# Kernel optimization log

Measured on AMD Instinct MI355X. Metric: run time of the kernel, lower is better.

## Reference

```python
import jax, jax.numpy as jnp
import numpy as np

B, S, D = 1, 4096, 512
QK_DIM, N_HEADS = 512, 8
HEAD_DIM = QK_DIM // N_HEADS


def setup_inputs() -> dict:
    key = jax.random.key(0)
    ks = jax.random.split(key, 9)
    s_in = 1.0 / np.sqrt(D)
    s_v = 1.0 / np.sqrt(QK_DIM)
    return {
        "x": jax.random.normal(ks[0], (B, S, D), dtype=jnp.float32),
        # torch nn.Linear convention: weight (out_features, in_features)
        "Wq": jax.random.uniform(ks[1], (QK_DIM, D), jnp.float32, -s_in, s_in),
        "bq": jax.random.uniform(ks[2], (QK_DIM,), jnp.float32, -s_in, s_in),
        "Wk": jax.random.uniform(ks[3], (QK_DIM, D), jnp.float32, -s_in, s_in),
        "bk": jax.random.uniform(ks[4], (QK_DIM,), jnp.float32, -s_in, s_in),
        "Wv": jax.random.uniform(ks[5], (QK_DIM, D), jnp.float32, -s_in, s_in),
        "bv": jax.random.uniform(ks[6], (QK_DIM,), jnp.float32, -s_in, s_in),
        "Wo": jax.random.uniform(ks[7], (D, QK_DIM), jnp.float32, -s_v, s_v),
        "bo": jax.random.uniform(ks[8], (D,), jnp.float32, -s_v, s_v),
    }


def reference(x, Wq, bq, Wk, bk, Wv, bv, Wo, bo):
    # Faithful to source: tokens flattened over batch*seq before head split.
    n = x.shape[0] * x.shape[1]  # B*S
    Q = (x @ Wq.T + bq).reshape(n, N_HEADS, HEAD_DIM).transpose(1, 0, 2)  # (H, N, hd)
    K = (x @ Wk.T + bk).reshape(n, N_HEADS, HEAD_DIM).transpose(1, 0, 2)
    V = (x @ Wv.T + bv).reshape(n, N_HEADS, HEAD_DIM).transpose(1, 0, 2)
    scores = jnp.einsum("hnd,hmd->hnm", Q, K) / np.sqrt(HEAD_DIM).astype(np.float32)
    attn = jax.nn.softmax(scores, axis=-1)                # (H, N, N) materialized
    ctx = jnp.einsum("hnm,hmd->hnd", attn, V)             # (H, N, hd)
    ctx = ctx.transpose(1, 0, 2).reshape(n, QK_DIM)       # (N, qk_dim)
    return ctx @ Wo.T + bo                                # (N, input_dim)
```

## Files before the change

kernel.cpp:

```cpp
#include <hip/hip_runtime.h>
#include <math.h>

#define N_TOK 4096
#define DMODEL 512
#define NH 8
#define HD 64

typedef __attribute__((ext_vector_type(4))) float f32x4;
typedef __attribute__((ext_vector_type(8))) _Float16 f16x8;
typedef __attribute__((ext_vector_type(4))) _Float16 f16x4;

#define MFMA16(A, B, C) __builtin_amdgcn_mfma_f32_16x16x32_f16(A, B, C, 0, 0, 0)

__global__ __launch_bounds__(256) void cast_x(const float* __restrict__ x,
                                              _Float16* __restrict__ X16) {
    int i = (blockIdx.x * 256 + threadIdx.x) * 8;
    f32x4 a = *(const f32x4*)&x[i];
    f32x4 b = *(const f32x4*)&x[i + 4];
    f16x8 o = {(_Float16)a[0], (_Float16)a[1], (_Float16)a[2], (_Float16)a[3],
               (_Float16)b[0], (_Float16)b[1], (_Float16)b[2], (_Float16)b[3]};
    *(f16x8*)&X16[i] = o;
}

__global__ __launch_bounds__(768) void qkv_gemm(const _Float16* __restrict__ X16,
                                                const float* __restrict__ Wq,
                                                const float* __restrict__ bq,
                                                const float* __restrict__ Wk,
                                                const float* __restrict__ bk,
                                                const float* __restrict__ Wv,
                                                const float* __restrict__ bv,
                                                _Float16* __restrict__ Q16,
                                                _Float16* __restrict__ K16,
                                                _Float16* __restrict__ VT16) {
    __shared__ __align__(16) _Float16 smem[46080];
    _Float16* AsB = smem;
    _Float16* WsB = smem + 18432;

    int t = threadIdx.x;
    int w = t >> 6, l = t & 63, quad = l >> 4, ln = l & 15;
    int z = w >> 2, ww = w & 3;
    int n0 = blockIdx.x * 128, o0 = blockIdx.y * 64;
    int h = o0 >> 6;

    const float* biasz = (z == 0) ? bq : (z == 1) ? bk : bv;

    f32x4 acc[2][4] = {};

    bool isA = (t < 256);
    int asr = t >> 3, asc = (t & 7) * 8;
    int tt = t - 256;
    int wr = tt >> 3, wc = (tt & 7) * 8;

    const _Float16* Abase = X16 + (size_t)n0 * DMODEL;
    const float* W0 = Wq + (size_t)o0 * DMODEL;
    const float* W1 = Wk + (size_t)o0 * DMODEL;
    const float* W2 = Wv + (size_t)o0 * DMODEL;

    f16x8 pa[4];
    f32x4 pw[3][2];
    if (isA) {
#pragma unroll
        for (int r = 0; r < 4; r++)
            pa[r] = *(const f16x8*)&Abase[(size_t)(asr + r * 32) * DMODEL + asc];
    } else {
        pw[0][0] = *(const f32x4*)&W0[(size_t)wr * DMODEL + wc];
        pw[0][1] = *(const f32x4*)&W0[(size_t)wr * DMODEL + wc + 4];
        pw[1][0] = *(const f32x4*)&W1[(size_t)wr * DMODEL + wc];
        pw[1][1] = *(const f32x4*)&W1[(size_t)wr * DMODEL + wc + 4];
        pw[2][0] = *(const f32x4*)&W2[(size_t)wr * DMODEL + wc];
        pw[2][1] = *(const f32x4*)&W2[(size_t)wr * DMODEL + wc + 4];
    }

    for (int it = 0; it < 8; it++) {
        int p = it & 1;
        if (isA) {
#pragma unroll
            for (int r = 0; r < 4; r++)
                *(f16x8*)&AsB[(size_t)(p * 128 + asr + r * 32) * 72 + asc] = pa[r];
        } else {
#pragma unroll
            for (int zt = 0; zt < 3; zt++) {
                f16x8 wv_ = {(_Float16)pw[zt][0][0], (_Float16)pw[zt][0][1],
                             (_Float16)pw[zt][0][2], (_Float16)pw[zt][0][3],
                             (_Float16)pw[zt][1][0], (_Float16)pw[zt][1][1],
                             (_Float16)pw[zt][1][2], (_Float16)pw[zt][1][3]};
                *(f16x8*)&WsB[(size_t)((p * 3 + zt) * 64 + wr) * 72 + wc] = wv_;
            }
        }
        __syncthreads();

        int k1 = (it + 1) * 64;
        if (k1 < DMODEL) {
            if (isA) {
#pragma unroll
                for (int r = 0; r < 4; r++)
                    pa[r] = *(const f16x8*)&Abase[(size_t)(asr + r * 32) * DMODEL + k1 + asc];
            } else {
                pw[0][0] = *(const f32x4*)&W0[(size_t)wr * DMODEL + k1 + wc];
                pw[0][1] = *(const f32x4*)&W0[(size_t)wr * DMODEL + k1 + wc + 4];
                pw[1][0] = *(const f32x4*)&W1[(size_t)wr * DMODEL + k1 + wc];
                pw[1][1] = *(const f32x4*)&W1[(size_t)wr * DMODEL + k1 + wc + 4];
                pw[2][0] = *(const f32x4*)&W2[(size_t)wr * DMODEL + k1 + wc];
                pw[2][1] = *(const f32x4*)&W2[(size_t)wr * DMODEL + k1 + wc + 4];
            }
        }

#pragma unroll
        for (int ks = 0; ks < 2; ks++) {
            f16x8 af0 = *(const f16x8*)&AsB[(size_t)(p * 128 + ww * 32 + ln) * 72 +
                                            ks * 32 + quad * 8];
            f16x8 af1 = *(const f16x8*)&AsB[(size_t)(p * 128 + ww * 32 + 16 + ln) * 72 +
                                            ks * 32 + quad * 8];
#pragma unroll
            for (int c = 0; c < 4; c++) {
                f16x8 bf = *(const f16x8*)&WsB[(size_t)((p * 3 + z) * 64 + c * 16 + ln) * 72 +
                                               ks * 32 + quad * 8];
                acc[0][c] = MFMA16(af0, bf, acc[0][c]);
                acc[1][c] = MFMA16(af1, bf, acc[1][c]);
            }
        }
    }

    __syncthreads();

    const float QS = 0.125f * 1.44269504088896340736f;
    _Float16* Qs = smem;
    _Float16* Ksep = smem + 9216;
    _Float16* Vt = smem + 18432;

    if (z < 2) {
        _Float16* st = (z == 0) ? Qs : Ksep;
        float sc_ = (z == 0) ? QS : 1.0f;
#pragma unroll
        for (int c = 0; c < 4; c++) {
            float bv_ = biasz[o0 + c * 16 + ln];
#pragma unroll
            for (int rt = 0; rt < 2; rt++)
#pragma unroll
                for (int i = 0; i < 4; i++) {
                    int lr = ww * 32 + rt * 16 + quad * 4 + i;
                    st[(size_t)lr * 72 + c * 16 + ln] =
                        (_Float16)((acc[rt][c][i] + bv_) * sc_);
                }
        }
    } else {
#pragma unroll
        for (int c = 0; c < 4; c++) {
            float bv_ = biasz[o0 + c * 16 + ln];
#pragma unroll
            for (int rt = 0; rt < 2; rt++)
#pragma unroll
                for (int i = 0; i < 4; i++) {
                    int np = (ww >> 1) * 64 + (quad * 4 + i) * 4 + (ww & 1) * 2 + rt;
                    Vt[(size_t)(c * 16 + ln) * 136 + np] = (_Float16)(acc[rt][c][i] + bv_);
                }
        }
    }
    __syncthreads();

    if (t < 256) {
#pragma unroll
        for (int k = 0; k < 4; k++) {
            int row = k * 32 + (t >> 3), col = (t & 7) * 8;
            *(f16x8*)&Q16[((size_t)h * N_TOK + n0 + row) * HD + col] =
                *(const f16x8*)&Qs[(size_t)row * 72 + col];
        }
    } else if (t < 512) {
        int u = t - 256;
#pragma unroll
        for (int k = 0; k < 4; k++) {
            int row = k * 32 + (u >> 3), col = (u & 7) * 8;
            *(f16x8*)&K16[((size_t)h * N_TOK + n0 + row) * HD + col] =
                *(const f16x8*)&Ksep[(size_t)row * 72 + col];
        }
    } else {
        int u = t - 512;
#pragma unroll
        for (int k = 0; k < 4; k++) {
            int d = k * 16 + (u >> 4), col = (u & 15) * 8;
            *(f16x8*)&VT16[((size_t)h * HD + d) * N_TOK + n0 + col] =
                *(const f16x8*)&Vt[(size_t)d * 136 + col];
        }
    }
}

__global__ __launch_bounds__(1024) void flash_mfma(const _Float16* __restrict__ Q16,
                                                   const _Float16* __restrict__ K16,
                                                   const _Float16* __restrict__ VT16,
                                                   _Float16* __restrict__ OP,
                                                   float* __restrict__ LS) {
    __shared__ __align__(16) _Float16 Ks[2][64][72];
    __shared__ __align__(16) _Float16 Vs[2][64][72];
    __shared__ __align__(16) _Float16 Ps[16][32][72];

    int t = threadIdx.x;
    int w = t >> 6, l = t & 63, quad = l >> 4, ln = l & 15;
    int bid = blockIdx.x;
    int h = bid & 7;
    int qt = (bid >> 3) & 7;
    int s = bid >> 6;
    int q0 = qt * 512 + w * 32;
    int m_start = s * 1024;

    f16x8 qf[2][2];
#pragma unroll
    for (int rt = 0; rt < 2; rt++) {
        const _Float16* qp = &Q16[((size_t)h * N_TOK + q0 + rt * 16 + ln) * HD + quad * 8];
        qf[rt][0] = *(const f16x8*)qp;
        qf[rt][1] = *(const f16x8*)(qp + 32);
    }

    f32x4 oacc[2][4] = {};
    f32x4 lsum[2] = {};

    const _Float16* kbase = K16 + (size_t)h * N_TOK * HD;
    const _Float16* vbase = VT16 + (size_t)h * HD * N_TOK;
    int g = t >> 9, tt = t & 511;
    int srow = tt >> 3, scol = (tt & 7) * 8;

    f16x8 pkv;
    if (g == 0)
        pkv = *(const f16x8*)(kbase + (size_t)(m_start + srow) * HD + scol);
    else
        pkv = *(const f16x8*)(vbase + (size_t)srow * N_TOK + m_start + scol);

    for (int it = 0; it < 16; it++) {
        int m0 = m_start + it * 64;
        int p = it & 1;
        if (g == 0)
            *(f16x8*)&Ks[p][srow][scol] = pkv;
        else
            *(f16x8*)&Vs[p][srow][scol] = pkv;
        __syncthreads();

        if (it < 15) {
            int m1 = m0 + 64;
            if (g == 0)
                pkv = *(const f16x8*)(kbase + (size_t)(m1 + srow) * HD + scol);
            else
                pkv = *(const f16x8*)(vbase + (size_t)srow * N_TOK + m1 + scol);
        }

        f16x8 kb[4][2];
#pragma unroll
        for (int c = 0; c < 4; c++) {
            kb[c][0] = *(const f16x8*)&Ks[p][c * 16 + ln][quad * 8];
            kb[c][1] = *(const f16x8*)&Ks[p][c * 16 + ln][32 + quad * 8];
        }
#pragma unroll
        for (int rt = 0; rt < 2; rt++) {
            f32x4 sacc[4] = {};
#pragma unroll
            for (int c = 0; c < 4; c++) {
                sacc[c] = MFMA16(qf[rt][0], kb[c][0], sacc[c]);
                sacc[c] = MFMA16(qf[rt][1], kb[c][1], sacc[c]);
            }
#pragma unroll
            for (int i = 0; i < 4; i++) {
                float p0 = __builtin_exp2f(sacc[0][i]);
                float p1 = __builtin_exp2f(sacc[1][i]);
                float p2 = __builtin_exp2f(sacc[2][i]);
                float p3 = __builtin_exp2f(sacc[3][i]);
                lsum[rt][i] += (p0 + p1) + (p2 + p3);
                f16x4 pvv = {(_Float16)p0, (_Float16)p1, (_Float16)p2, (_Float16)p3};
                *(f16x4*)&Ps[w][rt * 16 + quad * 4 + i][ln * 4] = pvv;
            }
        }
        f16x8 vb[4][2];
#pragma unroll
        for (int c = 0; c < 4; c++) {
            vb[c][0] = *(const f16x8*)&Vs[p][c * 16 + ln][quad * 8];
            vb[c][1] = *(const f16x8*)&Vs[p][c * 16 + ln][32 + quad * 8];
        }
#pragma unroll
        for (int rt = 0; rt < 2; rt++) {
            f16x8 a0 = *(const f16x8*)&Ps[w][rt * 16 + ln][quad * 8];
            f16x8 a1 = *(const f16x8*)&Ps[w][rt * 16 + ln][32 + quad * 8];
#pragma unroll
            for (int c = 0; c < 4; c++) {
                oacc[rt][c] = MFMA16(a0, vb[c][0], oacc[rt][c]);
                oacc[rt][c] = MFMA16(a1, vb[c][1], oacc[rt][c]);
            }
        }
    }

#pragma unroll
    for (int d = 1; d < 16; d <<= 1)
#pragma unroll
        for (int rt = 0; rt < 2; rt++)
#pragma unroll
            for (int i = 0; i < 4; i++) lsum[rt][i] += __shfl_xor(lsum[rt][i], d, 64);

    _Float16* obase = OP + (size_t)s * N_TOK * DMODEL;
#pragma unroll
    for (int rt = 0; rt < 2; rt++)
#pragma unroll
        for (int c = 0; c < 4; c++)
#pragma unroll
            for (int i = 0; i < 4; i++) {
                int r = q0 + rt * 16 + quad * 4 + i;
                obase[(size_t)r * DMODEL + h * HD + c * 16 + ln] = (_Float16)oacc[rt][c][i];
            }
    if (ln == 0) {
#pragma unroll
        for (int rt = 0; rt < 2; rt++)
#pragma unroll
            for (int i = 0; i < 4; i++) {
                int r = q0 + rt * 16 + quad * 4 + i;
                LS[((size_t)s * NH + h) * N_TOK + r] = lsum[rt][i];
            }
    }
}

__global__ __launch_bounds__(512) void out_gemm(const _Float16* __restrict__ OP,
                                                const float* __restrict__ LS,
                                                const float* __restrict__ Wo,
                                                const float* __restrict__ bo,
                                                float* __restrict__ out) {
    __shared__ __align__(16) _Float16 smem[27648];
    _Float16* AsB = smem;
    _Float16* WsB = smem + 18432;

    int t = threadIdx.x;
    int w = t >> 6, l = t & 63, quad = l >> 4, ln = l & 15;
    int n0 = blockIdx.x * 128, o0 = blockIdx.y * 64;
    int sr = t >> 2, sc = (t & 3) * 16;
    int wr = t >> 3, wc = (t & 7) * 8;
    const size_t PSTR = (size_t)N_TOK * DMODEL;

    f32x4 acc[4] = {};

    const float* Wbase = Wo + (size_t)o0 * DMODEL;

    f16x8 pa[4][2];
    float lt;
    f32x4 pw0, pw1;
    {
        size_t base = (size_t)(n0 + sr) * DMODEL + sc;
#pragma unroll
        for (int s_ = 0; s_ < 4; s_++) {
            pa[s_][0] = *(const f16x8*)&OP[s_ * PSTR + base];
            pa[s_][1] = *(const f16x8*)&OP[s_ * PSTR + base + 8];
        }
        const float* ls = LS + n0 + sr;
        lt = (ls[0] + ls[NH * N_TOK]) + (ls[2 * NH * N_TOK] + ls[3 * NH * N_TOK]);
        pw0 = *(const f32x4*)&Wbase[(size_t)wr * DMODEL + wc];
        pw1 = *(const f32x4*)&Wbase[(size_t)wr * DMODEL + wc + 4];
    }

    for (int it = 0; it < 8; it++) {
        int p = it & 1;
        {
            float inv = 1.0f / lt;
            f16x8 s0, s1;
#pragma unroll
            for (int j = 0; j < 8; j++) {
                s0[j] = (_Float16)(
                    ((((float)pa[0][0][j] + (float)pa[1][0][j]) +
                      ((float)pa[2][0][j] + (float)pa[3][0][j]))) * inv);
                s1[j] = (_Float16)(
                    ((((float)pa[0][1][j] + (float)pa[1][1][j]) +
                      ((float)pa[2][1][j] + (float)pa[3][1][j]))) * inv);
            }
            *(f16x8*)&AsB[(size_t)(p * 128 + sr) * 72 + sc] = s0;
            *(f16x8*)&AsB[(size_t)(p * 128 + sr) * 72 + sc + 8] = s1;
            f16x8 wv_ = {(_Float16)pw0[0], (_Float16)pw0[1], (_Float16)pw0[2],
                         (_Float16)pw0[3], (_Float16)pw1[0], (_Float16)pw1[1],
                         (_Float16)pw1[2], (_Float16)pw1[3]};
            *(f16x8*)&WsB[(size_t)(p * 64 + wr) * 72 + wc] = wv_;
        }
        __syncthreads();

        int k1 = (it + 1) * 64;
        if (k1 < DMODEL) {
            int h1 = k1 >> 6;
            size_t base = (size_t)(n0 + sr) * DMODEL + k1 + sc;
#pragma unroll
            for (int s_ = 0; s_ < 4; s_++) {
                pa[s_][0] = *(const f16x8*)&OP[s_ * PSTR + base];
                pa[s_][1] = *(const f16x8*)&OP[s_ * PSTR + base + 8];
            }
            const float* ls = LS + (size_t)h1 * N_TOK + n0 + sr;
            lt = (ls[0] + ls[NH * N_TOK]) + (ls[2 * NH * N_TOK] + ls[3 * NH * N_TOK]);
            pw0 = *(const f32x4*)&Wbase[(size_t)wr * DMODEL + k1 + wc];
            pw1 = *(const f32x4*)&Wbase[(size_t)wr * DMODEL + k1 + wc + 4];
        }

#pragma unroll
        for (int ks = 0; ks < 2; ks++) {
            f16x8 af = *(const f16x8*)&AsB[(size_t)(p * 128 + w * 16 + ln) * 72 +
                                           ks * 32 + quad * 8];
#pragma unroll
            for (int c = 0; c < 4; c++) {
                f16x8 bf = *(const f16x8*)&WsB[(size_t)(p * 64 + c * 16 + ln) * 72 +
                                               ks * 32 + quad * 8];
                acc[c] = MFMA16(af, bf, acc[c]);
            }
        }
    }

#pragma unroll
    for (int c = 0; c < 4; c++) {
        float bv_ = bo[o0 + c * 16 + ln];
#pragma unroll
        for (int i = 0; i < 4; i++) {
            int r = n0 + w * 16 + quad * 4 + i;
            out[(size_t)r * DMODEL + o0 + c * 16 + ln] = acc[c][i] + bv_;
        }
    }
}

extern "C" void kernel_launch(void* const* d_in, const int* in_sizes, int n_in,
                              void* d_out, int out_size, void* d_ws, size_t ws_size,
                              hipStream_t stream) {
    const float* x  = (const float*)d_in[0];
    const float* Wq = (const float*)d_in[1];
    const float* bq = (const float*)d_in[2];
    const float* Wk = (const float*)d_in[3];
    const float* bk = (const float*)d_in[4];
    const float* Wv = (const float*)d_in[5];
    const float* bv = (const float*)d_in[6];
    const float* Wo = (const float*)d_in[7];
    const float* bo = (const float*)d_in[8];
    float* out = (float*)d_out;

    char* ws = (char*)d_ws;
    _Float16* X16  = (_Float16*)(ws);
    _Float16* Q16  = (_Float16*)(ws + (4u << 20));
    _Float16* K16  = (_Float16*)(ws + (8u << 20));
    _Float16* VT16 = (_Float16*)(ws + (12u << 20));
    _Float16* OP   = (_Float16*)(ws + (16u << 20));
    float*    LSp  = (float*)   (ws + (32u << 20));

    cast_x<<<1024, 256, 0, stream>>>(x, X16);

    qkv_gemm<<<dim3(32, 8), 768, 0, stream>>>(X16, Wq, bq, Wk, bk, Wv, bv,
                                              Q16, K16, VT16);

    flash_mfma<<<dim3(256), 1024, 0, stream>>>(Q16, K16, VT16, OP, LSp);

    out_gemm<<<dim3(32, 8), 512, 0, stream>>>(OP, LSp, Wo, bo, out);
}
```

Before: 154.3 us.

## Swizzle flash-attention LDS tiles and halve block size to 512 threads

Replaces the padded LDS arrays (row stride 72) with dense 64-wide tiles that use an XOR swizzle on the column, aiming to avoid bank conflicts without the padding. Each block now runs 8 waves over 256 query rows instead of 16 waves over 512, so there are twice as many blocks, with launch bounds of 512 threads and 4 blocks per CU. Each loader thread now fetches two f16x8 vectors. The smaller shared footprint and blocks are meant to raise occupancy and help latency hiding, but each block now loads K/V tiles for half as many queries, which doubles the total K/V traffic.

```diff
diff --git a/kernel.cpp b/kernel.cpp
--- a/kernel.cpp
+++ b/kernel.cpp
@@ -184,22 +184,24 @@
     }
 }
 
-__global__ __launch_bounds__(1024) void flash_mfma(const _Float16* __restrict__ Q16,
-                                                   const _Float16* __restrict__ K16,
-                                                   const _Float16* __restrict__ VT16,
-                                                   _Float16* __restrict__ OP,
-                                                   float* __restrict__ LS) {
-    __shared__ __align__(16) _Float16 Ks[2][64][72];
-    __shared__ __align__(16) _Float16 Vs[2][64][72];
-    __shared__ __align__(16) _Float16 Ps[16][32][72];
+#define SWZ(r, c) (((r) * 64) + ((c) ^ (((r) & 7) << 3)))
+
+__global__ __launch_bounds__(512, 4) void flash_mfma(const _Float16* __restrict__ Q16,
+                                                     const _Float16* __restrict__ K16,
+                                                     const _Float16* __restrict__ VT16,
+                                                     _Float16* __restrict__ OP,
+                                                     float* __restrict__ LS) {
+    __shared__ __align__(16) _Float16 Ks[2][64 * 64];
+    __shared__ __align__(16) _Float16 Vs[2][64 * 64];
+    __shared__ __align__(16) _Float16 Ps[8][32 * 64];
 
     int t = threadIdx.x;
     int w = t >> 6, l = t & 63, quad = l >> 4, ln = l & 15;
     int bid = blockIdx.x;
     int h = bid & 7;
-    int qt = (bid >> 3) & 7;
-    int s = bid >> 6;
-    int q0 = qt * 512 + w * 32;
+    int qt = (bid >> 3) & 15;
+    int s = bid >> 7;
+    int q0 = qt * 256 + w * 32;
     int m_start = s * 1024;
 
     f16x8 qf[2][2];
@@ -215,37 +217,47 @@
 
     const _Float16* kbase = K16 + (size_t)h * N_TOK * HD;
     const _Float16* vbase = VT16 + (size_t)h * HD * N_TOK;
-    int g = t >> 9, tt = t & 511;
-    int srow = tt >> 3, scol = (tt & 7) * 8;
-
-    f16x8 pkv;
-    if (g == 0)
-        pkv = *(const f16x8*)(kbase + (size_t)(m_start + srow) * HD + scol);
-    else
-        pkv = *(const f16x8*)(vbase + (size_t)srow * N_TOK + m_start + scol);
+    int g = t >> 8, tt = t & 255;
+    int srow = tt >> 2, scol = (tt & 3) * 16;
+
+    f16x8 pk0, pk1;
+    if (g == 0) {
+        const _Float16* src = kbase + (size_t)(m_start + srow) * HD + scol;
+        pk0 = *(const f16x8*)src;
+        pk1 = *(const f16x8*)(src + 8);
+    } else {
+        const _Float16* src = vbase + (size_t)srow * N_TOK + m_start + scol;
+        pk0 = *(const f16x8*)src;
+        pk1 = *(const f16x8*)(src + 8);
+    }
 
     for (int it = 0; it < 16; it++) {
-        int m0 = m_start + it * 64;
         int p = it & 1;
-        if (g == 0)
-            *(f16x8*)&Ks[p][srow][scol] = pkv;
-        else
-            *(f16x8*)&Vs[p][srow][scol] = pkv;
+        {
+            _Float16* dst = (g == 0) ? &Ks[p][0] : &Vs[p][0];
+            *(f16x8*)&dst[SWZ(srow, scol)] = pk0;
+            *(f16x8*)&dst[SWZ(srow, scol + 8)] = pk1;
+        }
         __syncthreads();
 
         if (it < 15) {
-            int m1 = m0 + 64;
-            if (g == 0)
-                pkv = *(const f16x8*)(kbase + (size_t)(m1 + srow) * HD + scol);
-            else
-                pkv = *(const f16x8*)(vbase + (size_t)srow * N_TOK + m1 + scol);
+            int m1 = m_start + (it + 1) * 64;
+            if (g == 0) {
+                const _Float16* src = kbase + (size_t)(m1 + srow) * HD + scol;
+                pk0 = *(const f16x8*)src;
+                pk1 = *(const f16x8*)(src + 8);
+            } else {
+                const _Float16* src = vbase + (size_t)srow * N_TOK + m1 + scol;
+                pk0 = *(const f16x8*)src;
+                pk1 = *(const f16x8*)(src + 8);
+            }
         }
 
         f16x8 kb[4][2];
 #pragma unroll
         for (int c = 0; c < 4; c++) {
-            kb[c][0] = *(const f16x8*)&Ks[p][c * 16 + ln][quad * 8];
-            kb[c][1] = *(const f16x8*)&Ks[p][c * 16 + ln][32 + quad * 8];
+            kb[c][0] = *(const f16x8*)&Ks[p][SWZ(c * 16 + ln, quad * 8)];
+            kb[c][1] = *(const f16x8*)&Ks[p][SWZ(c * 16 + ln, 32 + quad * 8)];
         }
 #pragma unroll
         for (int rt = 0; rt < 2; rt++) {
@@ -263,19 +275,19 @@
                 float p3 = __builtin_exp2f(sacc[3][i]);
                 lsum[rt][i] += (p0 + p1) + (p2 + p3);
                 f16x4 pvv = {(_Float16)p0, (_Float16)p1, (_Float16)p2, (_Float16)p3};
-                *(f16x4*)&Ps[w][rt * 16 + quad * 4 + i][ln * 4] = pvv;
+                *(f16x4*)&Ps[w][SWZ(rt * 16 + quad * 4 + i, ln * 4)] = pvv;
             }
         }
         f16x8 vb[4][2];
 #pragma unroll
         for (int c = 0; c < 4; c++) {
-            vb[c][0] = *(const f16x8*)&Vs[p][c * 16 + ln][quad * 8];
-            vb[c][1] = *(const f16x8*)&Vs[p][c * 16 + ln][32 + quad * 8];
+            vb[c][0] = *(const f16x8*)&Vs[p][SWZ(c * 16 + ln, quad * 8)];
+            vb[c][1] = *(const f16x8*)&Vs[p][SWZ(c * 16 + ln, 32 + quad * 8)];
         }
 #pragma unroll
         for (int rt = 0; rt < 2; rt++) {
-            f16x8 a0 = *(const f16x8*)&Ps[w][rt * 16 + ln][quad * 8];
-            f16x8 a1 = *(const f16x8*)&Ps[w][rt * 16 + ln][32 + quad * 8];
+            f16x8 a0 = *(const f16x8*)&Ps[w][SWZ(rt * 16 + ln, quad * 8)];
+            f16x8 a1 = *(const f16x8*)&Ps[w][SWZ(rt * 16 + ln, 32 + quad * 8)];
 #pragma unroll
             for (int c = 0; c < 4; c++) {
                 oacc[rt][c] = MFMA16(a0, vb[c][0], oacc[rt][c]);
@@ -437,7 +449,7 @@
     qkv_gemm<<<dim3(32, 8), 768, 0, stream>>>(X16, Wq, bq, Wk, bk, Wv, bv,
                                               Q16, K16, VT16);
 
-    flash_mfma<<<dim3(256), 1024, 0, stream>>>(Q16, K16, VT16, OP, LSp);
+    flash_mfma<<<dim3(512), 512, 0, stream>>>(Q16, K16, VT16, OP, LSp);
 
     out_gemm<<<dim3(32, 8), 512, 0, stream>>>(OP, LSp, Wo, bo, out);
 }
```

Result: slower. 171.0 us (+10.8%).
